# Kernel tuning notes

Measured on AMD Instinct MI355X. Metric: run time of the kernel, lower is better.

## Reference

```python
import jax, jax.numpy as jnp
import numpy as np

S, B, H, N = 512, 32, 512, 131072  # seq_len, batch, hidden_dim, num candidate spans
MAX_STEP = 20  # max_length


def setup_inputs() -> dict:
    key = jax.random.key(0)
    ks = jax.random.split(key, 8)
    hidden = jax.random.normal(ks[0], (S, B, 2 * H), dtype=jnp.float32)
    span_bids = jax.random.randint(ks[1], (N,), 0, B, dtype=jnp.int32)
    # begin in [1, S-1-MAX_STEP-1] so that begin-1>=0 and end=begin+step <= S-1
    span_begins = jax.random.randint(ks[2], (N,), 1, S - MAX_STEP - 2, dtype=jnp.int32)
    steps = jax.random.randint(ks[3], (N,), 2, MAX_STEP + 1, dtype=jnp.int32)
    span_ends = span_begins + steps
    span_flags = jax.random.randint(ks[4], (N,), 0, 2, dtype=jnp.int32)
    span_weights = jax.random.uniform(ks[5], (N,), dtype=jnp.float32)
    W1 = jax.random.normal(ks[6], (2 * H, H), dtype=jnp.float32) / np.sqrt(2.0 * H)
    b1 = jnp.zeros((H,), dtype=jnp.float32)
    W2 = jax.random.normal(ks[7], (H, 1), dtype=jnp.float32) / np.sqrt(float(H))
    b2 = jnp.zeros((1,), dtype=jnp.float32)
    return {"hidden": hidden, "span_bids": span_bids, "span_begins": span_begins,
            "span_ends": span_ends, "span_flags": span_flags, "span_weights": span_weights,
            "W1": W1, "b1": b1, "W2": W2, "b2": b2}


def reference(hidden, span_bids, span_begins, span_ends, span_flags, span_weights, W1, b1, W2, b2):
    h = W2.shape[0]  # hidden_dim
    # vectorized _span_embed: fwd diff on first half, bwd diff on second half
    fwd = hidden[span_ends - 1, span_bids, :h] - hidden[span_begins - 1, span_bids, :h]
    bwd = hidden[span_begins, span_bids, h:] - hidden[span_ends, span_bids, h:]
    feats = jnp.concatenate([fwd, bwd], axis=-1)  # [N, 2H]
    z = jnp.maximum(feats @ W1 + b1, 0.0)
    p = jax.nn.sigmoid(z @ W2 + b2)[:, 0]  # [N]
    targets = (span_flags == 1).astype(p.dtype)
    n_pos = jnp.sum(targets)
    n_tot = jnp.asarray(targets.shape[0], p.dtype)
    scale = 2.0 * n_pos / n_tot  # negative weights scaled by 2*P/(P+N)
    w_eff = jnp.where(span_flags == 1, span_weights, span_weights * scale)
    pc = jnp.clip(p, 1e-7, 1.0 - 1e-7)
    bce = -(targets * jnp.log(pc) + (1.0 - targets) * jnp.log(1.0 - pc))
    loss = jnp.mean(w_eff * bce)
    return loss
```

## Files before the change

### kernel.cpp

```cpp
#include <hip/hip_runtime.h>
#include <hip/hip_bf16.h>


typedef float f32x4 __attribute__((ext_vector_type(4)));
typedef float f32x2 __attribute__((ext_vector_type(2)));
typedef __bf16 bf16x8 __attribute__((ext_vector_type(8)));

__device__ __forceinline__ unsigned short f2bf(float f) {
  unsigned int u = __float_as_uint(f);
  u += 0x7fffu + ((u >> 16) & 1u);
  return (unsigned short)(u >> 16);
}
__device__ __forceinline__ float bf2f(unsigned int lo16) {
  return __uint_as_float(lo16 << 16);
}

__global__ void w1_transpose(const float* __restrict__ W1, unsigned short* __restrict__ W1t) {
  __shared__ float tile[32][33];
  int k0 = blockIdx.x * 32, n0 = blockIdx.y * 32;
  int tx = threadIdx.x, ty = threadIdx.y;
#pragma unroll
  for (int r = 0; r < 4; ++r)
    tile[ty + r * 8][tx] = W1[(k0 + ty + r * 8) * 512 + n0 + tx];
  __syncthreads();
#pragma unroll
  for (int r = 0; r < 4; ++r)
    W1t[(n0 + ty + r * 8) * 1024 + k0 + tx] = f2bf(tile[tx][ty + r * 8]);
}

__global__ __launch_bounds__(256) void proj_gemm(
    const float* __restrict__ hidden,
    const unsigned short* __restrict__ w1t,
    unsigned char* __restrict__ Wq) {
  __shared__ __align__(16) char smem[35328];
  unsigned short* Ab = (unsigned short*)smem;
  unsigned short* Bb = (unsigned short*)(smem + 2560);
  unsigned short* Eb = (unsigned short*)smem;

  const int t = threadIdx.x;
  const int lane = t & 63;
  const int w = t >> 6;
  const int r0 = blockIdx.x << 5;
  const int hk = blockIdx.y << 9;

  f32x4 acc[2][8];
#pragma unroll
  for (int i = 0; i < 2; ++i)
#pragma unroll
    for (int j = 0; j < 8; ++j) acc[i][j] = (f32x4){0.f, 0.f, 0.f, 0.f};

  const int ar = t >> 3;
  const int akc = (t & 7) << 2;
  const float* agp = hidden + (r0 + ar) * 1024 + hk + akc;

  int boff[8];
#pragma unroll
  for (int q = 0; q < 8; ++q) {
    int n = (w << 7) + (q << 4) + (lane >> 2);
    int sc = (lane & 3) ^ ((n >> 1) & 3);
    boff[q] = n * 1024 + hk + (sc << 3);
  }

  for (int it = 0; it < 16; ++it) {
    const int k0 = it << 5;
#pragma unroll
    for (int q = 0; q < 8; ++q) {
      const unsigned short* gp = w1t + boff[q] + k0;
      unsigned short* lp = &Bb[((w << 7) + (q << 4)) << 5];
      __builtin_amdgcn_global_load_lds(
          (const __attribute__((address_space(1))) void*)gp,
          (__attribute__((address_space(3))) void*)lp, 16, 0, 0);
    }
    {
      float4 a = *(const float4*)(agp + k0);
      uint2 pk;
      pk.x = (unsigned)f2bf(a.x) | ((unsigned)f2bf(a.y) << 16);
      pk.y = (unsigned)f2bf(a.z) | ((unsigned)f2bf(a.w) << 16);
      *(uint2*)((char*)Ab + ar * 80 + akc * 2) = pk;
    }
    __syncthreads();

    bf16x8 af[2], bfr[8];
#pragma unroll
    for (int mt = 0; mt < 2; ++mt) {
      int row = (mt << 4) + (lane & 15);
      af[mt] = *(const bf16x8*)((const char*)Ab + row * 80 + ((lane >> 4) << 4));
    }
#pragma unroll
    for (int nt = 0; nt < 8; ++nt) {
      int n = (w << 7) + (nt << 4) + (lane & 15);
      int cs = (lane >> 4) ^ ((n >> 1) & 3);
      bfr[nt] = *(const bf16x8*)((const char*)Bb + n * 64 + (cs << 4));
    }
#pragma unroll
    for (int mt = 0; mt < 2; ++mt)
#pragma unroll
      for (int nt = 0; nt < 8; ++nt)
        acc[mt][nt] = __builtin_amdgcn_mfma_f32_16x16x32_bf16(af[mt], bfr[nt],
                                                              acc[mt][nt], 0, 0, 0);
    __syncthreads();
  }

#pragma unroll
  for (int mt = 0; mt < 2; ++mt)
#pragma unroll
    for (int r = 0; r < 4; ++r) {
      int rr = (mt << 4) + ((lane >> 4) << 2) + r;
#pragma unroll
      for (int nt = 0; nt < 8; ++nt)
        Eb[((w << 5) + rr) * 136 + (nt << 4) + (lane & 15)] = f2bf(acc[mt][nt][r]);
    }
#pragma unroll
  for (int i = 0; i < 8; ++i) {
    int task = (i << 6) + lane;
    int rr = task >> 4;
    int ck = task & 15;
    uint4 v = *(const uint4*)&Eb[((w << 5) + rr) * 136 + (ck << 3)];
    float f0 = bf2f(v.x & 0xffff), f1 = bf2f(v.x >> 16);
    float f2 = bf2f(v.y & 0xffff), f3 = bf2f(v.y >> 16);
    float f4 = bf2f(v.z & 0xffff), f5 = bf2f(v.z >> 16);
    float f6 = bf2f(v.w & 0xffff), f7 = bf2f(v.w >> 16);
    uint2 o;
    o.x = __builtin_amdgcn_cvt_pk_fp8_f32(f0, f1, 0, false);
    o.x = __builtin_amdgcn_cvt_pk_fp8_f32(f2, f3, o.x, true);
    o.y = __builtin_amdgcn_cvt_pk_fp8_f32(f4, f5, 0, false);
    o.y = __builtin_amdgcn_cvt_pk_fp8_f32(f6, f7, o.y, true);
    int grow = r0 + rr;
    int col = (w << 7) + (ck << 3);
    if (hk == 0) {
      *(uint2*)(Wq + (grow << 10) + col) = o;
    } else if (grow >= 32) {
      *(uint2*)(Wq + ((grow - 32) << 10) + 512 + col) = o;
    }
  }
}

#define SPB 64
__global__ __launch_bounds__(256) void span_eval(
    const unsigned char* __restrict__ Wq,
    const int* __restrict__ bids, const int* __restrict__ begins,
    const int* __restrict__ ends, const int* __restrict__ flags,
    const float* __restrict__ weights,
    const float* __restrict__ b1, const float* __restrict__ w2,
    const float* __restrict__ b2, float* __restrict__ partials) {
  __shared__ int oB[SPB], oE[SPB], sfl[SPB];
  __shared__ float swt[SPB];
  __shared__ float red[4][3];
  const int t = threadIdx.x;
  const int lane = t & 63;
  const int w = t >> 6;
  const int h = lane >> 5;
  const int hl = lane & 31;
  const int sbase = blockIdx.x * SPB;

  if (t < SPB) {
    int s = sbase + t;
    int b = bids[s], bg = begins[s], en = ends[s];
    oB[t] = (((bg - 1) << 5) + b) << 10;
    oE[t] = (((en - 1) << 5) + b) << 10;
    sfl[t] = flags[s];
    swt[t] = weights[s];
  }
  __syncthreads();

  const int sp0 = ((w << 1) + h) << 3;
  const int c0 = hl << 4;
  float b1v[16], w2v[16];
#pragma unroll
  for (int q = 0; q < 4; ++q) {
    float4 bv = *(const float4*)(b1 + c0 + (q << 2));
    float4 wv = *(const float4*)(w2 + c0 + (q << 2));
    b1v[(q << 2) + 0] = bv.x; b1v[(q << 2) + 1] = bv.y;
    b1v[(q << 2) + 2] = bv.z; b1v[(q << 2) + 3] = bv.w;
    w2v[(q << 2) + 0] = wv.x; w2v[(q << 2) + 1] = wv.y;
    w2v[(q << 2) + 2] = wv.z; w2v[(q << 2) + 3] = wv.w;
  }

  auto dec = [](unsigned int v, float* f) {
    f32x2 a = __builtin_amdgcn_cvt_pk_f32_fp8(v, false);
    f32x2 b = __builtin_amdgcn_cvt_pk_f32_fp8(v, true);
    f[0] = a[0]; f[1] = a[1]; f[2] = b[0]; f[3] = b[1];
  };

  uint4 BU[3], BV[3], EU[3], EV[3];
  auto ld = [&](int slot, int j) {
    int ob = oB[sp0 + j], oe = oE[sp0 + j];
    BU[slot] = *(const uint4*)(Wq + ob + c0);
    BV[slot] = *(const uint4*)(Wq + ob + 512 + c0);
    EU[slot] = *(const uint4*)(Wq + oe + c0);
    EV[slot] = *(const uint4*)(Wq + oe + 512 + c0);
  };
  ld(0, 0); ld(1, 1); ld(2, 2);

  float mylogit = 0.f;
#pragma unroll
  for (int j = 0; j < 8; ++j) {
    const int slot = j % 3;
    float buf[16], bvf[16], euf[16], evf[16];
    dec(BU[slot].x, buf); dec(BU[slot].y, buf + 4);
    dec(BU[slot].z, buf + 8); dec(BU[slot].w, buf + 12);
    dec(BV[slot].x, bvf); dec(BV[slot].y, bvf + 4);
    dec(BV[slot].z, bvf + 8); dec(BV[slot].w, bvf + 12);
    dec(EU[slot].x, euf); dec(EU[slot].y, euf + 4);
    dec(EU[slot].z, euf + 8); dec(EU[slot].w, euf + 12);
    dec(EV[slot].x, evf); dec(EV[slot].y, evf + 4);
    dec(EV[slot].z, evf + 8); dec(EV[slot].w, evf + 12);
    if (j + 3 < 8) ld(slot, j + 3);
    float sv = 0.f;
#pragma unroll
    for (int k = 0; k < 16; ++k) {
      float zp = euf[k] - buf[k] + bvf[k] - evf[k] + b1v[k];
      sv += fmaxf(zp, 0.f) * w2v[k];
    }
    sv += __shfl_xor(sv, 1);
    sv += __shfl_xor(sv, 2);
    sv += __shfl_xor(sv, 4);
    sv += __shfl_xor(sv, 8);
    sv += __shfl_xor(sv, 16);
    if (hl == j) mylogit = sv;
  }

  mylogit = __shfl(mylogit, ((lane & 8) << 2) + (lane & 7));

  float pos_t = 0.f, neg_t = 0.f, cnt_t = 0.f;
  if (lane < 16) {
    int sl = (w << 4) + lane;
    float logit = mylogit + b2[0];
    float p = 1.f / (1.f + expf(-logit));
    p = fminf(fmaxf(p, 1e-7f), 1.f - 1e-7f);
    int fl = sfl[sl];
    float bce = (fl == 1) ? -logf(p) : -logf(1.f - p);
    float term = swt[sl] * bce;
    pos_t = (fl == 1) ? term : 0.f;
    neg_t = (fl == 1) ? 0.f : term;
    cnt_t = (fl == 1) ? 1.f : 0.f;
  }
#pragma unroll
  for (int off = 1; off < 64; off <<= 1) {
    pos_t += __shfl_xor(pos_t, off);
    neg_t += __shfl_xor(neg_t, off);
    cnt_t += __shfl_xor(cnt_t, off);
  }
  if (lane == 0) { red[w][0] = pos_t; red[w][1] = neg_t; red[w][2] = cnt_t; }
  __syncthreads();
  if (t == 0) {
    partials[(blockIdx.x << 2) + 0] = red[0][0] + red[1][0] + red[2][0] + red[3][0];
    partials[(blockIdx.x << 2) + 1] = red[0][1] + red[1][1] + red[2][1] + red[3][1];
    partials[(blockIdx.x << 2) + 2] = red[0][2] + red[1][2] + red[2][2] + red[3][2];
  }
}

__global__ void finalize(const float* __restrict__ parts, int nblk,
                         float* __restrict__ out, int nspans) {
  __shared__ float sp[4], sn[4], sc[4];
  float P = 0.f, Ng = 0.f, C = 0.f;
  for (int i = threadIdx.x; i < nblk; i += 256) {
    P += parts[(i << 2) + 0];
    Ng += parts[(i << 2) + 1];
    C += parts[(i << 2) + 2];
  }
#pragma unroll
  for (int off = 1; off < 64; off <<= 1) {
    P += __shfl_xor(P, off);
    Ng += __shfl_xor(Ng, off);
    C += __shfl_xor(C, off);
  }
  int w = threadIdx.x >> 6;
  if ((threadIdx.x & 63) == 0) { sp[w] = P; sn[w] = Ng; sc[w] = C; }
  __syncthreads();
  if (threadIdx.x == 0) {
    P = sp[0] + sp[1] + sp[2] + sp[3];
    Ng = sn[0] + sn[1] + sn[2] + sn[3];
    C = sc[0] + sc[1] + sc[2] + sc[3];
    float scale = 2.f * C / (float)nspans;
    out[0] = (P + scale * Ng) / (float)nspans;
  }
}

extern "C" void kernel_launch(void* const* d_in, const int* in_sizes, int n_in,
                              void* d_out, int out_size, void* d_ws, size_t ws_size,
                              hipStream_t stream) {
  const float* hidden = (const float*)d_in[0];
  const int* bids     = (const int*)d_in[1];
  const int* begins   = (const int*)d_in[2];
  const int* ends     = (const int*)d_in[3];
  const int* flags    = (const int*)d_in[4];
  const float* weights = (const float*)d_in[5];
  const float* W1 = (const float*)d_in[6];
  const float* b1 = (const float*)d_in[7];
  const float* W2 = (const float*)d_in[8];
  const float* b2 = (const float*)d_in[9];
  float* out = (float*)d_out;
  const int nspans = in_sizes[1];
  const int nblk = nspans / SPB;

  float* partials = (float*)d_ws;
  unsigned short* W1t = (unsigned short*)((char*)d_ws + (1 << 18));
  unsigned char* Wq = (unsigned char*)((char*)d_ws + (2 << 20));

  w1_transpose<<<dim3(32, 16), dim3(32, 8), 0, stream>>>(W1, W1t);
  proj_gemm<<<dim3(512, 2), 256, 0, stream>>>(hidden, W1t, Wq);
  span_eval<<<nblk, 256, 0, stream>>>(Wq, bids, begins, ends, flags, weights,
                                      b1, W2, b2, partials);
  finalize<<<1, 256, 0, stream>>>(partials, nblk, out, nspans);
}
```

Measured before the change: 196.8 us.

## Load GEMM operands straight to registers with 64-row tiles and A prefetch

The projection GEMM no longer stages A and B tiles through LDS with barriers. Each wave now loads its MFMA fragments of W1t directly from global memory and register-prefetches the next fp32 hidden chunk. The M tile per block doubles to 64 rows, halving the grid, and the epilogue runs in two passes through a per-wave LDS buffer. This removes the two __syncthreads per k-step and the LDS round trip, at the cost of more registers (acc 4x8), redundant per-wave global B loads that must be served from cache, and possibly lower occupancy.

Result: slower. 207.5 us (+5.5%).

```diff
diff --git a/kernel.cpp b/kernel.cpp
--- a/kernel.cpp
+++ b/kernel.cpp
@@ -28,109 +28,108 @@
     W1t[(n0 + ty + r * 8) * 1024 + k0 + tx] = f2bf(tile[tx][ty + r * 8]);
 }
 
-__global__ __launch_bounds__(256) void proj_gemm(
+__global__ __launch_bounds__(256, 2) void proj_gemm(
     const float* __restrict__ hidden,
     const unsigned short* __restrict__ w1t,
     unsigned char* __restrict__ Wq) {
-  __shared__ __align__(16) char smem[35328];
-  unsigned short* Ab = (unsigned short*)smem;
-  unsigned short* Bb = (unsigned short*)(smem + 2560);
-  unsigned short* Eb = (unsigned short*)smem;
+  __shared__ __align__(16) unsigned short Eb[4][32][136];
 
   const int t = threadIdx.x;
   const int lane = t & 63;
   const int w = t >> 6;
-  const int r0 = blockIdx.x << 5;
+  const int r0 = blockIdx.x << 6;
   const int hk = blockIdx.y << 9;
-
-  f32x4 acc[2][8];
-#pragma unroll
-  for (int i = 0; i < 2; ++i)
+  const int kq = (lane >> 4) << 3;
+
+  f32x4 acc[4][8];
+#pragma unroll
+  for (int i = 0; i < 4; ++i)
 #pragma unroll
     for (int j = 0; j < 8; ++j) acc[i][j] = (f32x4){0.f, 0.f, 0.f, 0.f};
 
-  const int ar = t >> 3;
-  const int akc = (t & 7) << 2;
-  const float* agp = hidden + (r0 + ar) * 1024 + hk + akc;
-
-  int boff[8];
-#pragma unroll
-  for (int q = 0; q < 8; ++q) {
-    int n = (w << 7) + (q << 4) + (lane >> 2);
-    int sc = (lane & 3) ^ ((n >> 1) & 3);
-    boff[q] = n * 1024 + hk + (sc << 3);
+  int aoff[4];
+#pragma unroll
+  for (int mt = 0; mt < 4; ++mt)
+    aoff[mt] = ((r0 + (mt << 4) + (lane & 15)) << 10) + hk + kq;
+  int boffn[8];
+#pragma unroll
+  for (int nt = 0; nt < 8; ++nt)
+    boffn[nt] = (((w << 7) + (nt << 4) + (lane & 15)) << 10) + hk + kq;
+
+  float4 a0n[4], a1n[4];
+#pragma unroll
+  for (int mt = 0; mt < 4; ++mt) {
+    const float4* p = (const float4*)(hidden + aoff[mt]);
+    a0n[mt] = p[0]; a1n[mt] = p[1];
   }
 
   for (int it = 0; it < 16; ++it) {
     const int k0 = it << 5;
-#pragma unroll
-    for (int q = 0; q < 8; ++q) {
-      const unsigned short* gp = w1t + boff[q] + k0;
-      unsigned short* lp = &Bb[((w << 7) + (q << 4)) << 5];
-      __builtin_amdgcn_global_load_lds(
-          (const __attribute__((address_space(1))) void*)gp,
-          (__attribute__((address_space(3))) void*)lp, 16, 0, 0);
-    }
-    {
-      float4 a = *(const float4*)(agp + k0);
-      uint2 pk;
-      pk.x = (unsigned)f2bf(a.x) | ((unsigned)f2bf(a.y) << 16);
-      pk.y = (unsigned)f2bf(a.z) | ((unsigned)f2bf(a.w) << 16);
-      *(uint2*)((char*)Ab + ar * 80 + akc * 2) = pk;
-    }
-    __syncthreads();
-
-    bf16x8 af[2], bfr[8];
-#pragma unroll
-    for (int mt = 0; mt < 2; ++mt) {
-      int row = (mt << 4) + (lane & 15);
-      af[mt] = *(const bf16x8*)((const char*)Ab + row * 80 + ((lane >> 4) << 4));
-    }
-#pragma unroll
-    for (int nt = 0; nt < 8; ++nt) {
-      int n = (w << 7) + (nt << 4) + (lane & 15);
-      int cs = (lane >> 4) ^ ((n >> 1) & 3);
-      bfr[nt] = *(const bf16x8*)((const char*)Bb + n * 64 + (cs << 4));
-    }
-#pragma unroll
-    for (int mt = 0; mt < 2; ++mt)
+    bf16x8 bfr[8];
+#pragma unroll
+    for (int nt = 0; nt < 8; ++nt)
+      bfr[nt] = *(const bf16x8*)(w1t + boffn[nt] + k0);
+    bf16x8 af[4];
+#pragma unroll
+    for (int mt = 0; mt < 4; ++mt) {
+      uint2 lo, hi;
+      lo.x = (unsigned)f2bf(a0n[mt].x) | ((unsigned)f2bf(a0n[mt].y) << 16);
+      lo.y = (unsigned)f2bf(a0n[mt].z) | ((unsigned)f2bf(a0n[mt].w) << 16);
+      hi.x = (unsigned)f2bf(a1n[mt].x) | ((unsigned)f2bf(a1n[mt].y) << 16);
+      hi.y = (unsigned)f2bf(a1n[mt].z) | ((unsigned)f2bf(a1n[mt].w) << 16);
+      uint4 pk = make_uint4(lo.x, lo.y, hi.x, hi.y);
+      af[mt] = *(bf16x8*)&pk;
+    }
+    if (it < 15) {
+#pragma unroll
+      for (int mt = 0; mt < 4; ++mt) {
+        const float4* p = (const float4*)(hidden + aoff[mt] + k0 + 32);
+        a0n[mt] = p[0]; a1n[mt] = p[1];
+      }
+    }
+#pragma unroll
+    for (int mt = 0; mt < 4; ++mt)
 #pragma unroll
       for (int nt = 0; nt < 8; ++nt)
         acc[mt][nt] = __builtin_amdgcn_mfma_f32_16x16x32_bf16(af[mt], bfr[nt],
                                                               acc[mt][nt], 0, 0, 0);
-    __syncthreads();
-  }
-
-#pragma unroll
-  for (int mt = 0; mt < 2; ++mt)
-#pragma unroll
-    for (int r = 0; r < 4; ++r) {
-      int rr = (mt << 4) + ((lane >> 4) << 2) + r;
-#pragma unroll
-      for (int nt = 0; nt < 8; ++nt)
-        Eb[((w << 5) + rr) * 136 + (nt << 4) + (lane & 15)] = f2bf(acc[mt][nt][r]);
-    }
-#pragma unroll
-  for (int i = 0; i < 8; ++i) {
-    int task = (i << 6) + lane;
-    int rr = task >> 4;
-    int ck = task & 15;
-    uint4 v = *(const uint4*)&Eb[((w << 5) + rr) * 136 + (ck << 3)];
-    float f0 = bf2f(v.x & 0xffff), f1 = bf2f(v.x >> 16);
-    float f2 = bf2f(v.y & 0xffff), f3 = bf2f(v.y >> 16);
-    float f4 = bf2f(v.z & 0xffff), f5 = bf2f(v.z >> 16);
-    float f6 = bf2f(v.w & 0xffff), f7 = bf2f(v.w >> 16);
-    uint2 o;
-    o.x = __builtin_amdgcn_cvt_pk_fp8_f32(f0, f1, 0, false);
-    o.x = __builtin_amdgcn_cvt_pk_fp8_f32(f2, f3, o.x, true);
-    o.y = __builtin_amdgcn_cvt_pk_fp8_f32(f4, f5, 0, false);
-    o.y = __builtin_amdgcn_cvt_pk_fp8_f32(f6, f7, o.y, true);
-    int grow = r0 + rr;
-    int col = (w << 7) + (ck << 3);
-    if (hk == 0) {
-      *(uint2*)(Wq + (grow << 10) + col) = o;
-    } else if (grow >= 32) {
-      *(uint2*)(Wq + ((grow - 32) << 10) + 512 + col) = o;
+  }
+
+#pragma unroll
+  for (int pass = 0; pass < 2; ++pass) {
+#pragma unroll
+    for (int mh = 0; mh < 2; ++mh) {
+      int mt = (pass << 1) + mh;
+#pragma unroll
+      for (int r = 0; r < 4; ++r) {
+        int rr = (mh << 4) + ((lane >> 4) << 2) + r;
+#pragma unroll
+        for (int nt = 0; nt < 8; ++nt)
+          Eb[w][rr][(nt << 4) + (lane & 15)] = f2bf(acc[mt][nt][r]);
+      }
+    }
+#pragma unroll
+    for (int i = 0; i < 8; ++i) {
+      int task = (i << 6) + lane;
+      int rr = task >> 4;
+      int ck = task & 15;
+      uint4 v = *(const uint4*)&Eb[w][rr][ck << 3];
+      float f0 = bf2f(v.x & 0xffff), f1 = bf2f(v.x >> 16);
+      float f2 = bf2f(v.y & 0xffff), f3 = bf2f(v.y >> 16);
+      float f4 = bf2f(v.z & 0xffff), f5 = bf2f(v.z >> 16);
+      float f6 = bf2f(v.w & 0xffff), f7 = bf2f(v.w >> 16);
+      uint2 o;
+      o.x = __builtin_amdgcn_cvt_pk_fp8_f32(f0, f1, 0, false);
+      o.x = __builtin_amdgcn_cvt_pk_fp8_f32(f2, f3, o.x, true);
+      o.y = __builtin_amdgcn_cvt_pk_fp8_f32(f4, f5, 0, false);
+      o.y = __builtin_amdgcn_cvt_pk_fp8_f32(f6, f7, o.y, true);
+      int grow = r0 + (pass << 5) + rr;
+      int col = (w << 7) + (ck << 3);
+      if (hk == 0) {
+        *(uint2*)(Wq + (grow << 10) + col) = o;
+      } else if (grow >= 32) {
+        *(uint2*)(Wq + ((grow - 32) << 10) + 512 + col) = o;
+      }
     }
   }
 }
@@ -299,7 +298,7 @@
   unsigned char* Wq = (unsigned char*)((char*)d_ws + (2 << 20));
 
   w1_transpose<<<dim3(32, 16), dim3(32, 8), 0, stream>>>(W1, W1t);
-  proj_gemm<<<dim3(512, 2), 256, 0, stream>>>(hidden, W1t, Wq);
+  proj_gemm<<<dim3(256, 2), 256, 0, stream>>>(hidden, W1t, Wq);
   span_eval<<<nblk, 256, 0, stream>>>(Wq, bids, begins, ends, flags, weights,
                                       b1, W2, b2, partials);
   finalize<<<1, 256, 0, stream>>>(partials, nblk, out, nspans);
```

## Merge both K-halves of projection GEMM into one block with full A tile in LDS

Applied to the files above, without the earlier changes.

Each block now converts its full 32x1024 row strip of hidden to bf16 once into LDS, then runs the two K-halves (forward and backward) back to back, so the grid shrinks from 512x2 to 512 blocks. B fragments are read straight from global memory (W1t, likely L2-resident) rather than staged through LDS with per-iteration barriers, and the K loops are fully unrolled. This removes the per-iteration syncs and the redundant hidden reads, at the cost of about 68KB of LDS per block, which limits occupancy and exposes the MFMAs to global-load latency on B.

Result: slower. 211.4 us (+7.4%).

```diff
diff --git a/kernel.cpp b/kernel.cpp
--- a/kernel.cpp
+++ b/kernel.cpp
@@ -28,20 +28,53 @@
     W1t[(n0 + ty + r * 8) * 1024 + k0 + tx] = f2bf(tile[tx][ty + r * 8]);
 }
 
-__global__ __launch_bounds__(256) void proj_gemm(
+#define APITCH 520
+__global__ __launch_bounds__(256, 2) void proj_gemm(
     const float* __restrict__ hidden,
     const unsigned short* __restrict__ w1t,
     unsigned char* __restrict__ Wq) {
-  __shared__ __align__(16) char smem[35328];
-  unsigned short* Ab = (unsigned short*)smem;
-  unsigned short* Bb = (unsigned short*)(smem + 2560);
-  unsigned short* Eb = (unsigned short*)smem;
+  __shared__ __align__(16) unsigned short smem[34048];
+  unsigned short* AU = smem;
+  unsigned short* AV = smem + 17408;
+  unsigned short* Eb = smem;
 
   const int t = threadIdx.x;
   const int lane = t & 63;
   const int w = t >> 6;
   const int r0 = blockIdx.x << 5;
-  const int hk = blockIdx.y << 9;
+  const int kq = (lane >> 4) << 3;
+
+  {
+    const int c16 = t & 63;
+    const int rsub = t >> 6;
+#pragma unroll 4
+    for (int p = 0; p < 8; ++p) {
+      int row = (p << 2) + rsub;
+      const float4* gp = (const float4*)(hidden + ((r0 + row) << 10) + (c16 << 4));
+      float4 f0 = gp[0], f1 = gp[1], f2 = gp[2], f3 = gp[3];
+      uint4 a, b;
+      a.x = (unsigned)f2bf(f0.x) | ((unsigned)f2bf(f0.y) << 16);
+      a.y = (unsigned)f2bf(f0.z) | ((unsigned)f2bf(f0.w) << 16);
+      a.z = (unsigned)f2bf(f1.x) | ((unsigned)f2bf(f1.y) << 16);
+      a.w = (unsigned)f2bf(f1.z) | ((unsigned)f2bf(f1.w) << 16);
+      b.x = (unsigned)f2bf(f2.x) | ((unsigned)f2bf(f2.y) << 16);
+      b.y = (unsigned)f2bf(f2.z) | ((unsigned)f2bf(f2.w) << 16);
+      b.z = (unsigned)f2bf(f3.x) | ((unsigned)f2bf(f3.y) << 16);
+      b.w = (unsigned)f2bf(f3.z) | ((unsigned)f2bf(f3.w) << 16);
+      unsigned short* dst = (c16 < 32) ? (AU + row * APITCH + (c16 << 4))
+                                       : (AV + row * APITCH + ((c16 - 32) << 4));
+      *(uint4*)dst = a;
+      *(uint4*)(dst + 8) = b;
+    }
+  }
+  __syncthreads();
+
+  int boffn[8];
+#pragma unroll
+  for (int nt = 0; nt < 8; ++nt)
+    boffn[nt] = (((w << 7) + (nt << 4) + (lane & 15)) << 10) + kq;
+
+  const int arow = lane & 15;
 
   f32x4 acc[2][8];
 #pragma unroll
@@ -49,57 +82,22 @@
 #pragma unroll
     for (int j = 0; j < 8; ++j) acc[i][j] = (f32x4){0.f, 0.f, 0.f, 0.f};
 
-  const int ar = t >> 3;
-  const int akc = (t & 7) << 2;
-  const float* agp = hidden + (r0 + ar) * 1024 + hk + akc;
-
-  int boff[8];
-#pragma unroll
-  for (int q = 0; q < 8; ++q) {
-    int n = (w << 7) + (q << 4) + (lane >> 2);
-    int sc = (lane & 3) ^ ((n >> 1) & 3);
-    boff[q] = n * 1024 + hk + (sc << 3);
-  }
-
+#pragma unroll
   for (int it = 0; it < 16; ++it) {
     const int k0 = it << 5;
-#pragma unroll
-    for (int q = 0; q < 8; ++q) {
-      const unsigned short* gp = w1t + boff[q] + k0;
-      unsigned short* lp = &Bb[((w << 7) + (q << 4)) << 5];
-      __builtin_amdgcn_global_load_lds(
-          (const __attribute__((address_space(1))) void*)gp,
-          (__attribute__((address_space(3))) void*)lp, 16, 0, 0);
-    }
-    {
-      float4 a = *(const float4*)(agp + k0);
-      uint2 pk;
-      pk.x = (unsigned)f2bf(a.x) | ((unsigned)f2bf(a.y) << 16);
-      pk.y = (unsigned)f2bf(a.z) | ((unsigned)f2bf(a.w) << 16);
-      *(uint2*)((char*)Ab + ar * 80 + akc * 2) = pk;
-    }
-    __syncthreads();
-
-    bf16x8 af[2], bfr[8];
-#pragma unroll
-    for (int mt = 0; mt < 2; ++mt) {
-      int row = (mt << 4) + (lane & 15);
-      af[mt] = *(const bf16x8*)((const char*)Ab + row * 80 + ((lane >> 4) << 4));
-    }
+    bf16x8 af0 = *(const bf16x8*)(AU + arow * APITCH + k0 + kq);
+    bf16x8 af1 = *(const bf16x8*)(AU + (16 + arow) * APITCH + k0 + kq);
+    bf16x8 bfr[8];
+#pragma unroll
+    for (int nt = 0; nt < 8; ++nt)
+      bfr[nt] = *(const bf16x8*)(w1t + boffn[nt] + k0);
 #pragma unroll
     for (int nt = 0; nt < 8; ++nt) {
-      int n = (w << 7) + (nt << 4) + (lane & 15);
-      int cs = (lane >> 4) ^ ((n >> 1) & 3);
-      bfr[nt] = *(const bf16x8*)((const char*)Bb + n * 64 + (cs << 4));
-    }
-#pragma unroll
-    for (int mt = 0; mt < 2; ++mt)
-#pragma unroll
-      for (int nt = 0; nt < 8; ++nt)
-        acc[mt][nt] = __builtin_amdgcn_mfma_f32_16x16x32_bf16(af[mt], bfr[nt],
-                                                              acc[mt][nt], 0, 0, 0);
-    __syncthreads();
-  }
+      acc[0][nt] = __builtin_amdgcn_mfma_f32_16x16x32_bf16(af0, bfr[nt], acc[0][nt], 0, 0, 0);
+      acc[1][nt] = __builtin_amdgcn_mfma_f32_16x16x32_bf16(af1, bfr[nt], acc[1][nt], 0, 0, 0);
+    }
+  }
+  __syncthreads();
 
 #pragma unroll
   for (int mt = 0; mt < 2; ++mt)
@@ -126,12 +124,57 @@
     o.y = __builtin_amdgcn_cvt_pk_fp8_f32(f4, f5, 0, false);
     o.y = __builtin_amdgcn_cvt_pk_fp8_f32(f6, f7, o.y, true);
     int grow = r0 + rr;
-    int col = (w << 7) + (ck << 3);
-    if (hk == 0) {
-      *(uint2*)(Wq + (grow << 10) + col) = o;
-    } else if (grow >= 32) {
-      *(uint2*)(Wq + ((grow - 32) << 10) + 512 + col) = o;
-    }
+    *(uint2*)(Wq + (grow << 10) + (w << 7) + (ck << 3)) = o;
+  }
+
+#pragma unroll
+  for (int i = 0; i < 2; ++i)
+#pragma unroll
+    for (int j = 0; j < 8; ++j) acc[i][j] = (f32x4){0.f, 0.f, 0.f, 0.f};
+
+#pragma unroll
+  for (int it = 0; it < 16; ++it) {
+    const int k0 = it << 5;
+    bf16x8 af0 = *(const bf16x8*)(AV + arow * APITCH + k0 + kq);
+    bf16x8 af1 = *(const bf16x8*)(AV + (16 + arow) * APITCH + k0 + kq);
+    bf16x8 bfr[8];
+#pragma unroll
+    for (int nt = 0; nt < 8; ++nt)
+      bfr[nt] = *(const bf16x8*)(w1t + boffn[nt] + 512 + k0);
+#pragma unroll
+    for (int nt = 0; nt < 8; ++nt) {
+      acc[0][nt] = __builtin_amdgcn_mfma_f32_16x16x32_bf16(af0, bfr[nt], acc[0][nt], 0, 0, 0);
+      acc[1][nt] = __builtin_amdgcn_mfma_f32_16x16x32_bf16(af1, bfr[nt], acc[1][nt], 0, 0, 0);
+    }
+  }
+
+#pragma unroll
+  for (int mt = 0; mt < 2; ++mt)
+#pragma unroll
+    for (int r = 0; r < 4; ++r) {
+      int rr = (mt << 4) + ((lane >> 4) << 2) + r;
+#pragma unroll
+      for (int nt = 0; nt < 8; ++nt)
+        Eb[((w << 5) + rr) * 136 + (nt << 4) + (lane & 15)] = f2bf(acc[mt][nt][r]);
+    }
+#pragma unroll
+  for (int i = 0; i < 8; ++i) {
+    int task = (i << 6) + lane;
+    int rr = task >> 4;
+    int ck = task & 15;
+    uint4 v = *(const uint4*)&Eb[((w << 5) + rr) * 136 + (ck << 3)];
+    float f0 = bf2f(v.x & 0xffff), f1 = bf2f(v.x >> 16);
+    float f2 = bf2f(v.y & 0xffff), f3 = bf2f(v.y >> 16);
+    float f4 = bf2f(v.z & 0xffff), f5 = bf2f(v.z >> 16);
+    float f6 = bf2f(v.w & 0xffff), f7 = bf2f(v.w >> 16);
+    uint2 o;
+    o.x = __builtin_amdgcn_cvt_pk_fp8_f32(f0, f1, 0, false);
+    o.x = __builtin_amdgcn_cvt_pk_fp8_f32(f2, f3, o.x, true);
+    o.y = __builtin_amdgcn_cvt_pk_fp8_f32(f4, f5, 0, false);
+    o.y = __builtin_amdgcn_cvt_pk_fp8_f32(f6, f7, o.y, true);
+    int grow = r0 + rr;
+    if (grow >= 32)
+      *(uint2*)(Wq + ((grow - 32) << 10) + 512 + (w << 7) + (ck << 3)) = o;
   }
 }
 
@@ -299,7 +342,7 @@
   unsigned char* Wq = (unsigned char*)((char*)d_ws + (2 << 20));
 
   w1_transpose<<<dim3(32, 16), dim3(32, 8), 0, stream>>>(W1, W1t);
-  proj_gemm<<<dim3(512, 2), 256, 0, stream>>>(hidden, W1t, Wq);
+  proj_gemm<<<512, 256, 0, stream>>>(hidden, W1t, Wq);
   span_eval<<<nblk, 256, 0, stream>>>(Wq, bids, begins, ends, flags, weights,
                                       b1, W2, b2, partials);
   finalize<<<1, 256, 0, stream>>>(partials, nblk, out, nspans);
```
